# Kernel optimization log

Hardware: AMD Instinct MI355X
Metric: run time of the kernel (lower is better)

## Reference

```python
import jax, jax.numpy as jnp
import numpy as np

B, H, S, D = 2, 16, 2048, 64

def setup_inputs() -> dict:
    key = jax.random.key(0)
    kq, kk, kv = jax.random.split(key, 3)
    Q = jax.random.normal(kq, (B, H, S, D), dtype=jnp.float32)
    K = jax.random.normal(kk, (B, H, S, D), dtype=jnp.float32)
    V = jax.random.normal(kv, (B, H, S, D), dtype=jnp.float32)
    return {"Q": Q, "K": K, "V": V}

def reference(Q, K, V):
    # scores: [B, H, S, S]
    scale = 1.0 / jnp.sqrt(jnp.asarray(Q.shape[-1], Q.dtype))
    scores = jnp.einsum('bhqd,bhkd->bhqk', Q, K) * scale
    probs = jax.nn.softmax(scores, axis=-1)
    out = jnp.einsum('bhqk,bhkd->bhqd', probs, V)
    return out
```

## Files before the change

kernel.cpp:

```cpp
#include <hip/hip_runtime.h>
#include <hip/hip_bf16.h>


#define Bn 2
#define Hn 16
#define Sn 2048
#define Dn 64
#define KP 72
#define OP 68

typedef __attribute__((ext_vector_type(8)))  short s16x8;
typedef __attribute__((ext_vector_type(16))) float f32x16;

__device__ __forceinline__ float fast_exp2(float x) {
#if __has_builtin(__builtin_amdgcn_exp2f)
    return __builtin_amdgcn_exp2f(x);
#else
    return exp2f(x);
#endif
}
__device__ __forceinline__ unsigned short f2bf(float f) {
    unsigned u = __float_as_uint(f);
    return (unsigned short)((u + 0x7fffu + ((u >> 16) & 1u)) >> 16);
}
__device__ __forceinline__ unsigned pack2bf(float lo, float hi) {
    return (unsigned)f2bf(lo) | ((unsigned)f2bf(hi) << 16);
}
__device__ __forceinline__ unsigned packtrunc(float lo, float hi) {
#if __has_builtin(__builtin_amdgcn_perm)
    return __builtin_amdgcn_perm(__float_as_uint(hi), __float_as_uint(lo),
                                 0x07060302u);
#else
    return (__float_as_uint(lo) >> 16) | (__float_as_uint(hi) & 0xffff0000u);
#endif
}
__device__ __forceinline__ s16x8 lds_frag(const unsigned short* p) {
    uint4 u = *(const uint4*)p;
    return __builtin_bit_cast(s16x8, u);
}
__device__ __forceinline__ s16x8 reg_frag(uint4 u) {
    return __builtin_bit_cast(s16x8, u);
}

__global__ __launch_bounds__(256)
void cast_kv2(const float* __restrict__ K, const float* __restrict__ V,
              unsigned short* __restrict__ Kb, unsigned short* __restrict__ Vt) {
    __shared__ unsigned short TK[64 * 72];
    __shared__ unsigned short TV[64 * 72];
    const int tid = threadIdx.x;
    const int bh  = blockIdx.x >> 5;
    const int kt  = blockIdx.x & 31;
    const int r = tid >> 2, cc = (tid & 3) * 16;

    const size_t rowbase = ((size_t)bh * Sn + (size_t)kt * 64 + r) * Dn + cc;
    {
        const float* ks = K + rowbase;
        #pragma unroll
        for (int i = 0; i < 2; ++i) {
            float4 f0 = *(const float4*)(ks + 8 * i);
            float4 f1 = *(const float4*)(ks + 8 * i + 4);
            uint4 w;
            w.x = pack2bf(f0.x, f0.y); w.y = pack2bf(f0.z, f0.w);
            w.z = pack2bf(f1.x, f1.y); w.w = pack2bf(f1.z, f1.w);
            *(uint4*)(TK + r * 72 + cc + 8 * i) = w;
        }
    }
    {
        const float* vs = V + rowbase;
        #pragma unroll
        for (int i = 0; i < 4; ++i) {
            float4 f = *(const float4*)(vs + 4 * i);
            const int d0 = cc + 4 * i;
            TV[(d0 + 0) * 72 + r] = f2bf(f.x);
            TV[(d0 + 1) * 72 + r] = f2bf(f.y);
            TV[(d0 + 2) * 72 + r] = f2bf(f.z);
            TV[(d0 + 3) * 72 + r] = f2bf(f.w);
        }
    }
    __syncthreads();
    unsigned short* kd = Kb + ((size_t)(bh * 32 + kt) * 8) * 512;
    unsigned short* vd = Vt + ((size_t)(bh * 32 + kt) * 8) * 512;
    #pragma unroll
    for (int i = 0; i < 2; ++i) {
        const int u = i * 256 + tid;
        const int c = u >> 6, lane = u & 63;
        const int l31 = lane & 31, hf = lane >> 5;
        const int sub = c >> 2, ks = c & 3;
        const int off = (sub * 32 + l31) * 72 + ks * 16 + hf * 8;
        *(uint4*)(kd + c * 512 + lane * 8) = *(const uint4*)(TK + off);
        *(uint4*)(vd + c * 512 + lane * 8) = *(const uint4*)(TV + off);
    }
}

__global__ __launch_bounds__(128, 2)
void attn_fwd_mfma4(const float* __restrict__ Q,
                    const unsigned short* __restrict__ Kb,
                    const unsigned short* __restrict__ Vt,
                    float* __restrict__ O) {
    __shared__ __align__(16) char smem[18432];
    unsigned short* PT = (unsigned short*)smem;
    float* ob = (float*)smem;
    float* lb = ob + 64 * OP;

    const int tid  = threadIdx.x;
    const int wave = tid >> 6;
    const int lane = tid & 63;
    const int l31  = lane & 31;
    const int half = lane >> 5;

    const int bh = blockIdx.x & 31;
    const int q0 = (blockIdx.x >> 5) * 64;

    const float* Qb = Q + ((size_t)bh * Sn + q0) * Dn;
    const float FCT = 0.18033688011112042f;

    s16x8 qf[2][4];
    #pragma unroll
    for (int s = 0; s < 2; ++s) {
        const float* qp = Qb + (size_t)(s * 32 + l31) * Dn;
        #pragma unroll
        for (int ks = 0; ks < 4; ++ks) {
            const int d0 = ks * 16 + half * 8;
            float4 f0 = *(const float4*)(qp + d0);
            float4 f1 = *(const float4*)(qp + d0 + 4);
            uint4 u;
            u.x = pack2bf(f0.x * FCT, f0.y * FCT);
            u.y = pack2bf(f0.z * FCT, f0.w * FCT);
            u.z = pack2bf(f1.x * FCT, f1.y * FCT);
            u.w = pack2bf(f1.z * FCT, f1.w * FCT);
            qf[s][ks] = __builtin_bit_cast(s16x8, u);
        }
    }

    f32x16 acc00, acc01, acc10, acc11;
    #pragma unroll
    for (int r = 0; r < 16; ++r) { acc00[r]=0.f; acc01[r]=0.f; acc10[r]=0.f; acc11[r]=0.f; }
    float l0 = 0.f, l1 = 0.f;

    const unsigned short* kbase =
        Kb + ((size_t)(bh * 32 + wave * 16) * 8) * 512 + (size_t)lane * 8;
    const unsigned short* vbase =
        Vt + ((size_t)(bh * 32 + wave * 16) * 8) * 512 + (size_t)lane * 8;

    unsigned short* ptw0 = PT + ((size_t)wave * 64 + l31) * KP;
    unsigned short* ptw1 = ptw0 + 32 * KP;

    uint4 kbuf[2][8], vv[8];
    #pragma unroll
    for (int c = 0; c < 8; ++c)
        kbuf[0][c] = *(const uint4*)(kbase + c * 512);

    #pragma unroll
    for (int t = 0; t < 16; ++t) {
        uint4* CUR = kbuf[t & 1];
        uint4* NXT = kbuf[(t + 1) & 1];
        #pragma unroll
        for (int c = 0; c < 8; ++c)
            vv[c] = *(const uint4*)(vbase + (size_t)(t * 8 + c) * 512);
        const int tk = (t < 15 ? t + 1 : 15);
        #pragma unroll
        for (int c = 0; c < 8; ++c)
            NXT[c] = *(const uint4*)(kbase + (size_t)(tk * 8 + c) * 512);

        #pragma unroll
        for (int s = 0; s < 2; ++s) {
            f32x16 c0, c1;
            #pragma unroll
            for (int r = 0; r < 16; ++r) { c0[r] = 0.f; c1[r] = 0.f; }
            __builtin_amdgcn_s_setprio(1);
            #pragma unroll
            for (int ks = 0; ks < 4; ++ks) {
                c0 = __builtin_amdgcn_mfma_f32_32x32x16_bf16(reg_frag(CUR[ks]),     qf[s][ks], c0, 0, 0, 0);
                c1 = __builtin_amdgcn_mfma_f32_32x32x16_bf16(reg_frag(CUR[4 + ks]), qf[s][ks], c1, 0, 0, 0);
            }
            __builtin_amdgcn_s_setprio(0);
            #pragma unroll
            for (int r = 0; r < 16; ++r) {
                c0[r] = fast_exp2(c0[r]);
                c1[r] = fast_exp2(c1[r]);
            }
            float a0 = 0.f, a1 = 0.f, a2 = 0.f, a3 = 0.f;
            #pragma unroll
            for (int r = 0; r < 16; r += 4) {
                a0 += c0[r] + c1[r];
                a1 += c0[r + 1] + c1[r + 1];
                a2 += c0[r + 2] + c1[r + 2];
                a3 += c0[r + 3] + c1[r + 3];
            }
            if (s == 0) l0 += (a0 + a1) + (a2 + a3);
            else        l1 += (a0 + a1) + (a2 + a3);

            unsigned short* ptw = s ? ptw1 : ptw0;
            #pragma unroll
            for (int g = 0; g < 4; ++g) {
                uint2 w0, w1;
                w0.x = packtrunc(c0[4 * g + 0], c0[4 * g + 1]);
                w0.y = packtrunc(c0[4 * g + 2], c0[4 * g + 3]);
                w1.x = packtrunc(c1[4 * g + 0], c1[4 * g + 1]);
                w1.y = packtrunc(c1[4 * g + 2], c1[4 * g + 3]);
                *(uint2*)(ptw + 8 * g + 4 * half)      = w0;
                *(uint2*)(ptw + 8 * g + 4 * half + 32) = w1;
            }
        }

        __builtin_amdgcn_s_setprio(1);
        #pragma unroll
        for (int ks = 0; ks < 4; ++ks) {
            const int off = ks * 16 + half * 8;
            s16x8 pf0 = lds_frag(ptw0 + off);
            s16x8 pf1 = lds_frag(ptw1 + off);
            s16x8 va  = reg_frag(vv[ks]);
            s16x8 vb  = reg_frag(vv[4 + ks]);
            acc00 = __builtin_amdgcn_mfma_f32_32x32x16_bf16(va, pf0, acc00, 0, 0, 0);
            acc01 = __builtin_amdgcn_mfma_f32_32x32x16_bf16(vb, pf0, acc01, 0, 0, 0);
            acc10 = __builtin_amdgcn_mfma_f32_32x32x16_bf16(va, pf1, acc10, 0, 0, 0);
            acc11 = __builtin_amdgcn_mfma_f32_32x32x16_bf16(vb, pf1, acc11, 0, 0, 0);
        }
        __builtin_amdgcn_s_setprio(0);
    }

    l0 += __shfl_xor(l0, 32, 64);
    l1 += __shfl_xor(l1, 32, 64);

    __syncthreads();
    if (wave == 0) {
        #pragma unroll
        for (int g = 0; g < 4; ++g) {
            const int d0 = 8 * g + 4 * half;
            float4 f;
            f.x = acc00[4*g+0]; f.y = acc00[4*g+1]; f.z = acc00[4*g+2]; f.w = acc00[4*g+3];
            *(float4*)(ob + l31 * OP + d0) = f;
            f.x = acc01[4*g+0]; f.y = acc01[4*g+1]; f.z = acc01[4*g+2]; f.w = acc01[4*g+3];
            *(float4*)(ob + l31 * OP + d0 + 32) = f;
            f.x = acc10[4*g+0]; f.y = acc10[4*g+1]; f.z = acc10[4*g+2]; f.w = acc10[4*g+3];
            *(float4*)(ob + (32 + l31) * OP + d0) = f;
            f.x = acc11[4*g+0]; f.y = acc11[4*g+1]; f.z = acc11[4*g+2]; f.w = acc11[4*g+3];
            *(float4*)(ob + (32 + l31) * OP + d0 + 32) = f;
        }
        if (half == 0) { lb[l31] = l0; lb[32 + l31] = l1; }
    }
    __syncthreads();
    if (wave == 1) {
        const float i0 = 1.0f / (l0 + lb[l31]);
        const float i1 = 1.0f / (l1 + lb[32 + l31]);
        #pragma unroll
        for (int g = 0; g < 4; ++g) {
            const int d0 = 8 * g + 4 * half;
            float4 f;
            float* p;
            p = ob + l31 * OP + d0;            f = *(float4*)p;
            f.x = (f.x + acc00[4*g+0]) * i0; f.y = (f.y + acc00[4*g+1]) * i0;
            f.z = (f.z + acc00[4*g+2]) * i0; f.w = (f.w + acc00[4*g+3]) * i0;
            *(float4*)p = f;
            p = ob + l31 * OP + d0 + 32;       f = *(float4*)p;
            f.x = (f.x + acc01[4*g+0]) * i0; f.y = (f.y + acc01[4*g+1]) * i0;
            f.z = (f.z + acc01[4*g+2]) * i0; f.w = (f.w + acc01[4*g+3]) * i0;
            *(float4*)p = f;
            p = ob + (32 + l31) * OP + d0;     f = *(float4*)p;
            f.x = (f.x + acc10[4*g+0]) * i1; f.y = (f.y + acc10[4*g+1]) * i1;
            f.z = (f.z + acc10[4*g+2]) * i1; f.w = (f.w + acc10[4*g+3]) * i1;
            *(float4*)p = f;
            p = ob + (32 + l31) * OP + d0 + 32; f = *(float4*)p;
            f.x = (f.x + acc11[4*g+0]) * i1; f.y = (f.y + acc11[4*g+1]) * i1;
            f.z = (f.z + acc11[4*g+2]) * i1; f.w = (f.w + acc11[4*g+3]) * i1;
            *(float4*)p = f;
        }
    }
    __syncthreads();
    float* op = O + ((size_t)bh * Sn + q0) * Dn;
    #pragma unroll
    for (int it = 0; it < 8; ++it) {
        const int idx = it * 128 + tid;
        const int r = idx >> 4, c4 = (idx & 15) * 4;
        *(float4*)(op + r * Dn + c4) = *(float4*)(ob + r * OP + c4);
    }
}

extern "C" void kernel_launch(void* const* d_in, const int* in_sizes, int n_in,
                              void* d_out, int out_size, void* d_ws, size_t ws_size,
                              hipStream_t stream) {
    const float* Q = (const float*)d_in[0];
    const float* K = (const float*)d_in[1];
    const float* V = (const float*)d_in[2];
    float* O = (float*)d_out;

    const size_t elems = (size_t)Bn * Hn * Sn * Dn;
    unsigned short* Kb = (unsigned short*)d_ws;
    unsigned short* Vt = Kb + elems;

    cast_kv2<<<dim3(Bn * Hn * (Sn / 64)), dim3(256), 0, stream>>>(K, V, Kb, Vt);
    attn_fwd_mfma4<<<dim3(Bn * Hn * (Sn / 64)), dim3(128), 0, stream>>>(Q, Kb, Vt, O);
}
```

Measured before the change: 130.9 us.

## Split key range across four waves per block with LDS reduction

Each block now runs four waves instead of two, and each wave handles one eighth of the key tiles instead of half. The partial outputs and row sums are reduced through a larger shared buffer: two staging buffers, pairwise adds, and a final combine-and-normalize during the store. The first score MFMA now takes a zero vector directly instead of a zero-initialized accumulator. The aim is more parallelism per query tile and shorter serial loops, at the cost of more shared memory, an extra reduction stage, and a tighter register budget from the launch bounds of 256 threads with 4 blocks.

```diff
diff --git a/kernel.cpp b/kernel.cpp
--- a/kernel.cpp
+++ b/kernel.cpp
@@ -92,15 +92,16 @@
     }
 }
 
-__global__ __launch_bounds__(128, 2)
+__global__ __launch_bounds__(256, 4)
 void attn_fwd_mfma4(const float* __restrict__ Q,
                     const unsigned short* __restrict__ Kb,
                     const unsigned short* __restrict__ Vt,
                     float* __restrict__ O) {
-    __shared__ __align__(16) char smem[18432];
+    __shared__ __align__(16) char smem[36864];
     unsigned short* PT = (unsigned short*)smem;
-    float* ob = (float*)smem;
-    float* lb = ob + 64 * OP;
+    float* ob0 = (float*)smem;
+    float* ob1 = ob0 + 64 * OP;
+    float* lb  = ob0 + 2 * 64 * OP;
 
     const int tid  = threadIdx.x;
     const int wave = tid >> 6;
@@ -132,15 +133,19 @@
         }
     }
 
+    f32x16 Z16;
+    #pragma unroll
+    for (int r = 0; r < 16; ++r) Z16[r] = 0.f;
+
     f32x16 acc00, acc01, acc10, acc11;
     #pragma unroll
     for (int r = 0; r < 16; ++r) { acc00[r]=0.f; acc01[r]=0.f; acc10[r]=0.f; acc11[r]=0.f; }
     float l0 = 0.f, l1 = 0.f;
 
     const unsigned short* kbase =
-        Kb + ((size_t)(bh * 32 + wave * 16) * 8) * 512 + (size_t)lane * 8;
+        Kb + ((size_t)(bh * 32 + wave * 8) * 8) * 512 + (size_t)lane * 8;
     const unsigned short* vbase =
-        Vt + ((size_t)(bh * 32 + wave * 16) * 8) * 512 + (size_t)lane * 8;
+        Vt + ((size_t)(bh * 32 + wave * 8) * 8) * 512 + (size_t)lane * 8;
 
     unsigned short* ptw0 = PT + ((size_t)wave * 64 + l31) * KP;
     unsigned short* ptw1 = ptw0 + 32 * KP;
@@ -151,25 +156,24 @@
         kbuf[0][c] = *(const uint4*)(kbase + c * 512);
 
     #pragma unroll
-    for (int t = 0; t < 16; ++t) {
+    for (int t = 0; t < 8; ++t) {
         uint4* CUR = kbuf[t & 1];
         uint4* NXT = kbuf[(t + 1) & 1];
         #pragma unroll
         for (int c = 0; c < 8; ++c)
             vv[c] = *(const uint4*)(vbase + (size_t)(t * 8 + c) * 512);
-        const int tk = (t < 15 ? t + 1 : 15);
+        const int tk = (t < 7 ? t + 1 : 7);
         #pragma unroll
         for (int c = 0; c < 8; ++c)
             NXT[c] = *(const uint4*)(kbase + (size_t)(tk * 8 + c) * 512);
 
         #pragma unroll
         for (int s = 0; s < 2; ++s) {
-            f32x16 c0, c1;
+            __builtin_amdgcn_s_setprio(1);
+            f32x16 c0 = __builtin_amdgcn_mfma_f32_32x32x16_bf16(reg_frag(CUR[0]), qf[s][0], Z16, 0, 0, 0);
+            f32x16 c1 = __builtin_amdgcn_mfma_f32_32x32x16_bf16(reg_frag(CUR[4]), qf[s][0], Z16, 0, 0, 0);
             #pragma unroll
-            for (int r = 0; r < 16; ++r) { c0[r] = 0.f; c1[r] = 0.f; }
-            __builtin_amdgcn_s_setprio(1);
-            #pragma unroll
-            for (int ks = 0; ks < 4; ++ks) {
+            for (int ks = 1; ks < 4; ++ks) {
                 c0 = __builtin_amdgcn_mfma_f32_32x32x16_bf16(reg_frag(CUR[ks]),     qf[s][ks], c0, 0, 0, 0);
                 c1 = __builtin_amdgcn_mfma_f32_32x32x16_bf16(reg_frag(CUR[4 + ks]), qf[s][ks], c1, 0, 0, 0);
             }
@@ -223,56 +227,64 @@
     l1 += __shfl_xor(l1, 32, 64);
 
     __syncthreads();
-    if (wave == 0) {
+    if (half == 0) {
+        lb[wave * 64 + l31]      = l0;
+        lb[wave * 64 + 32 + l31] = l1;
+    }
+    float* obw = (wave & 2) ? ob1 : ob0;
+    if (!(wave & 1)) {
         #pragma unroll
         for (int g = 0; g < 4; ++g) {
             const int d0 = 8 * g + 4 * half;
             float4 f;
             f.x = acc00[4*g+0]; f.y = acc00[4*g+1]; f.z = acc00[4*g+2]; f.w = acc00[4*g+3];
-            *(float4*)(ob + l31 * OP + d0) = f;
+            *(float4*)(obw + l31 * OP + d0) = f;
             f.x = acc01[4*g+0]; f.y = acc01[4*g+1]; f.z = acc01[4*g+2]; f.w = acc01[4*g+3];
-            *(float4*)(ob + l31 * OP + d0 + 32) = f;
+            *(float4*)(obw + l31 * OP + d0 + 32) = f;
             f.x = acc10[4*g+0]; f.y = acc10[4*g+1]; f.z = acc10[4*g+2]; f.w = acc10[4*g+3];
-            *(float4*)(ob + (32 + l31) * OP + d0) = f;
+            *(float4*)(obw + (32 + l31) * OP + d0) = f;
             f.x = acc11[4*g+0]; f.y = acc11[4*g+1]; f.z = acc11[4*g+2]; f.w = acc11[4*g+3];
-            *(float4*)(ob + (32 + l31) * OP + d0 + 32) = f;
-        }
-        if (half == 0) { lb[l31] = l0; lb[32 + l31] = l1; }
+            *(float4*)(obw + (32 + l31) * OP + d0 + 32) = f;
+        }
     }
     __syncthreads();
-    if (wave == 1) {
-        const float i0 = 1.0f / (l0 + lb[l31]);
-        const float i1 = 1.0f / (l1 + lb[32 + l31]);
+    if (wave & 1) {
         #pragma unroll
         for (int g = 0; g < 4; ++g) {
             const int d0 = 8 * g + 4 * half;
             float4 f;
             float* p;
-            p = ob + l31 * OP + d0;            f = *(float4*)p;
-            f.x = (f.x + acc00[4*g+0]) * i0; f.y = (f.y + acc00[4*g+1]) * i0;
-            f.z = (f.z + acc00[4*g+2]) * i0; f.w = (f.w + acc00[4*g+3]) * i0;
+            p = obw + l31 * OP + d0;            f = *(float4*)p;
+            f.x += acc00[4*g+0]; f.y += acc00[4*g+1];
+            f.z += acc00[4*g+2]; f.w += acc00[4*g+3];
             *(float4*)p = f;
-            p = ob + l31 * OP + d0 + 32;       f = *(float4*)p;
-            f.x = (f.x + acc01[4*g+0]) * i0; f.y = (f.y + acc01[4*g+1]) * i0;
-            f.z = (f.z + acc01[4*g+2]) * i0; f.w = (f.w + acc01[4*g+3]) * i0;
+            p = obw + l31 * OP + d0 + 32;       f = *(float4*)p;
+            f.x += acc01[4*g+0]; f.y += acc01[4*g+1];
+            f.z += acc01[4*g+2]; f.w += acc01[4*g+3];
             *(float4*)p = f;
-            p = ob + (32 + l31) * OP + d0;     f = *(float4*)p;
-            f.x = (f.x + acc10[4*g+0]) * i1; f.y = (f.y + acc10[4*g+1]) * i1;
-            f.z = (f.z + acc10[4*g+2]) * i1; f.w = (f.w + acc10[4*g+3]) * i1;
+            p = obw + (32 + l31) * OP + d0;     f = *(float4*)p;
+            f.x += acc10[4*g+0]; f.y += acc10[4*g+1];
+            f.z += acc10[4*g+2]; f.w += acc10[4*g+3];
             *(float4*)p = f;
-            p = ob + (32 + l31) * OP + d0 + 32; f = *(float4*)p;
-            f.x = (f.x + acc11[4*g+0]) * i1; f.y = (f.y + acc11[4*g+1]) * i1;
-            f.z = (f.z + acc11[4*g+2]) * i1; f.w = (f.w + acc11[4*g+3]) * i1;
+            p = obw + (32 + l31) * OP + d0 + 32; f = *(float4*)p;
+            f.x += acc11[4*g+0]; f.y += acc11[4*g+1];
+            f.z += acc11[4*g+2]; f.w += acc11[4*g+3];
             *(float4*)p = f;
         }
     }
     __syncthreads();
     float* op = O + ((size_t)bh * Sn + q0) * Dn;
     #pragma unroll
-    for (int it = 0; it < 8; ++it) {
-        const int idx = it * 128 + tid;
+    for (int it = 0; it < 4; ++it) {
+        const int idx = it * 256 + tid;
         const int r = idx >> 4, c4 = (idx & 15) * 4;
-        *(float4*)(op + r * Dn + c4) = *(float4*)(ob + r * OP + c4);
+        const float inv = 1.0f / (lb[r] + lb[64 + r] + lb[128 + r] + lb[192 + r]);
+        float4 a = *(float4*)(ob0 + r * OP + c4);
+        float4 b = *(float4*)(ob1 + r * OP + c4);
+        float4 f;
+        f.x = (a.x + b.x) * inv; f.y = (a.y + b.y) * inv;
+        f.z = (a.z + b.z) * inv; f.w = (a.w + b.w) * inv;
+        *(float4*)(op + r * Dn + c4) = f;
     }
 }
 
@@ -289,5 +301,5 @@
     unsigned short* Vt = Kb + elems;
 
     cast_kv2<<<dim3(Bn * Hn * (Sn / 64)), dim3(256), 0, stream>>>(K, V, Kb, Vt);
-    attn_fwd_mfma4<<<dim3(Bn * Hn * (Sn / 64)), dim3(128), 0, stream>>>(Q, Kb, Vt, O);
-}
+    attn_fwd_mfma4<<<dim3(Bn * Hn * (Sn / 64)), dim3(256), 0, stream>>>(Q, Kb, Vt, O);
+}
```

Measured after the change: 331.3 us. 2.53x slower.

## Halve query tile to 32 rows per block, doubling grid and occupancy

Applied to the files above, without the earlier changes.

Each block now handles 32 query rows instead of 64, so the grid doubles and per-block LDS and accumulator registers halve. Launch bounds are raised to allow 4 blocks per SM, and the K double-buffer prefetch is replaced by a per-iteration load. Normalisation moves into the final store loop. Each K/V tile loaded from memory now feeds half as many MFMAs, so global and L2 traffic for K/V doubles in exchange for more waves to hide latency.

```diff
diff --git a/kernel.cpp b/kernel.cpp
--- a/kernel.cpp
+++ b/kernel.cpp
@@ -92,15 +92,15 @@
     }
 }
 
-__global__ __launch_bounds__(128, 2)
+__global__ __launch_bounds__(128, 4)
 void attn_fwd_mfma4(const float* __restrict__ Q,
                     const unsigned short* __restrict__ Kb,
                     const unsigned short* __restrict__ Vt,
                     float* __restrict__ O) {
-    __shared__ __align__(16) char smem[18432];
+    __shared__ __align__(16) char smem[9216];
     unsigned short* PT = (unsigned short*)smem;
     float* ob = (float*)smem;
-    float* lb = ob + 64 * OP;
+    float* lb = ob + 32 * OP;
 
     const int tid  = threadIdx.x;
     const int wave = tid >> 6;
@@ -109,15 +109,14 @@
     const int half = lane >> 5;
 
     const int bh = blockIdx.x & 31;
-    const int q0 = (blockIdx.x >> 5) * 64;
+    const int q0 = (blockIdx.x >> 5) * 32;
 
     const float* Qb = Q + ((size_t)bh * Sn + q0) * Dn;
     const float FCT = 0.18033688011112042f;
 
-    s16x8 qf[2][4];
-    #pragma unroll
-    for (int s = 0; s < 2; ++s) {
-        const float* qp = Qb + (size_t)(s * 32 + l31) * Dn;
+    s16x8 qf[4];
+    {
+        const float* qp = Qb + (size_t)l31 * Dn;
         #pragma unroll
         for (int ks = 0; ks < 4; ++ks) {
             const int d0 = ks * 16 + half * 8;
@@ -128,151 +127,124 @@
             u.y = pack2bf(f0.z * FCT, f0.w * FCT);
             u.z = pack2bf(f1.x * FCT, f1.y * FCT);
             u.w = pack2bf(f1.z * FCT, f1.w * FCT);
-            qf[s][ks] = __builtin_bit_cast(s16x8, u);
-        }
-    }
-
-    f32x16 acc00, acc01, acc10, acc11;
-    #pragma unroll
-    for (int r = 0; r < 16; ++r) { acc00[r]=0.f; acc01[r]=0.f; acc10[r]=0.f; acc11[r]=0.f; }
-    float l0 = 0.f, l1 = 0.f;
+            qf[ks] = __builtin_bit_cast(s16x8, u);
+        }
+    }
+
+    f32x16 acc0, acc1;
+    #pragma unroll
+    for (int r = 0; r < 16; ++r) { acc0[r] = 0.f; acc1[r] = 0.f; }
+    float l0 = 0.f;
 
     const unsigned short* kbase =
         Kb + ((size_t)(bh * 32 + wave * 16) * 8) * 512 + (size_t)lane * 8;
     const unsigned short* vbase =
         Vt + ((size_t)(bh * 32 + wave * 16) * 8) * 512 + (size_t)lane * 8;
 
-    unsigned short* ptw0 = PT + ((size_t)wave * 64 + l31) * KP;
-    unsigned short* ptw1 = ptw0 + 32 * KP;
-
-    uint4 kbuf[2][8], vv[8];
-    #pragma unroll
-    for (int c = 0; c < 8; ++c)
-        kbuf[0][c] = *(const uint4*)(kbase + c * 512);
+    unsigned short* ptw = PT + ((size_t)(wave * 32 + l31)) * KP;
 
     #pragma unroll
     for (int t = 0; t < 16; ++t) {
-        uint4* CUR = kbuf[t & 1];
-        uint4* NXT = kbuf[(t + 1) & 1];
+        uint4 kk[8];
+        #pragma unroll
+        for (int c = 0; c < 8; ++c)
+            kk[c] = *(const uint4*)(kbase + (size_t)(t * 8 + c) * 512);
+
+        f32x16 c0, c1;
+        #pragma unroll
+        for (int r = 0; r < 16; ++r) { c0[r] = 0.f; c1[r] = 0.f; }
+        __builtin_amdgcn_s_setprio(1);
+        #pragma unroll
+        for (int ks = 0; ks < 4; ++ks) {
+            c0 = __builtin_amdgcn_mfma_f32_32x32x16_bf16(reg_frag(kk[ks]),     qf[ks], c0, 0, 0, 0);
+            c1 = __builtin_amdgcn_mfma_f32_32x32x16_bf16(reg_frag(kk[4 + ks]), qf[ks], c1, 0, 0, 0);
+        }
+        __builtin_amdgcn_s_setprio(0);
+
+        uint4 vv[8];
         #pragma unroll
         for (int c = 0; c < 8; ++c)
             vv[c] = *(const uint4*)(vbase + (size_t)(t * 8 + c) * 512);
-        const int tk = (t < 15 ? t + 1 : 15);
-        #pragma unroll
-        for (int c = 0; c < 8; ++c)
-            NXT[c] = *(const uint4*)(kbase + (size_t)(tk * 8 + c) * 512);
-
-        #pragma unroll
-        for (int s = 0; s < 2; ++s) {
-            f32x16 c0, c1;
-            #pragma unroll
-            for (int r = 0; r < 16; ++r) { c0[r] = 0.f; c1[r] = 0.f; }
-            __builtin_amdgcn_s_setprio(1);
-            #pragma unroll
-            for (int ks = 0; ks < 4; ++ks) {
-                c0 = __builtin_amdgcn_mfma_f32_32x32x16_bf16(reg_frag(CUR[ks]),     qf[s][ks], c0, 0, 0, 0);
-                c1 = __builtin_amdgcn_mfma_f32_32x32x16_bf16(reg_frag(CUR[4 + ks]), qf[s][ks], c1, 0, 0, 0);
-            }
-            __builtin_amdgcn_s_setprio(0);
-            #pragma unroll
-            for (int r = 0; r < 16; ++r) {
-                c0[r] = fast_exp2(c0[r]);
-                c1[r] = fast_exp2(c1[r]);
-            }
-            float a0 = 0.f, a1 = 0.f, a2 = 0.f, a3 = 0.f;
-            #pragma unroll
-            for (int r = 0; r < 16; r += 4) {
-                a0 += c0[r] + c1[r];
-                a1 += c0[r + 1] + c1[r + 1];
-                a2 += c0[r + 2] + c1[r + 2];
-                a3 += c0[r + 3] + c1[r + 3];
-            }
-            if (s == 0) l0 += (a0 + a1) + (a2 + a3);
-            else        l1 += (a0 + a1) + (a2 + a3);
-
-            unsigned short* ptw = s ? ptw1 : ptw0;
-            #pragma unroll
-            for (int g = 0; g < 4; ++g) {
-                uint2 w0, w1;
-                w0.x = packtrunc(c0[4 * g + 0], c0[4 * g + 1]);
-                w0.y = packtrunc(c0[4 * g + 2], c0[4 * g + 3]);
-                w1.x = packtrunc(c1[4 * g + 0], c1[4 * g + 1]);
-                w1.y = packtrunc(c1[4 * g + 2], c1[4 * g + 3]);
-                *(uint2*)(ptw + 8 * g + 4 * half)      = w0;
-                *(uint2*)(ptw + 8 * g + 4 * half + 32) = w1;
-            }
+
+        #pragma unroll
+        for (int r = 0; r < 16; ++r) {
+            c0[r] = fast_exp2(c0[r]);
+            c1[r] = fast_exp2(c1[r]);
+        }
+        float a0 = 0.f, a1 = 0.f, a2 = 0.f, a3 = 0.f;
+        #pragma unroll
+        for (int r = 0; r < 16; r += 4) {
+            a0 += c0[r] + c1[r];
+            a1 += c0[r + 1] + c1[r + 1];
+            a2 += c0[r + 2] + c1[r + 2];
+            a3 += c0[r + 3] + c1[r + 3];
+        }
+        l0 += (a0 + a1) + (a2 + a3);
+
+        #pragma unroll
+        for (int g = 0; g < 4; ++g) {
+            uint2 w0, w1;
+            w0.x = packtrunc(c0[4 * g + 0], c0[4 * g + 1]);
+            w0.y = packtrunc(c0[4 * g + 2], c0[4 * g + 3]);
+            w1.x = packtrunc(c1[4 * g + 0], c1[4 * g + 1]);
+            w1.y = packtrunc(c1[4 * g + 2], c1[4 * g + 3]);
+            *(uint2*)(ptw + 8 * g + 4 * half)      = w0;
+            *(uint2*)(ptw + 8 * g + 4 * half + 32) = w1;
         }
 
         __builtin_amdgcn_s_setprio(1);
         #pragma unroll
         for (int ks = 0; ks < 4; ++ks) {
             const int off = ks * 16 + half * 8;
-            s16x8 pf0 = lds_frag(ptw0 + off);
-            s16x8 pf1 = lds_frag(ptw1 + off);
-            s16x8 va  = reg_frag(vv[ks]);
-            s16x8 vb  = reg_frag(vv[4 + ks]);
-            acc00 = __builtin_amdgcn_mfma_f32_32x32x16_bf16(va, pf0, acc00, 0, 0, 0);
-            acc01 = __builtin_amdgcn_mfma_f32_32x32x16_bf16(vb, pf0, acc01, 0, 0, 0);
-            acc10 = __builtin_amdgcn_mfma_f32_32x32x16_bf16(va, pf1, acc10, 0, 0, 0);
-            acc11 = __builtin_amdgcn_mfma_f32_32x32x16_bf16(vb, pf1, acc11, 0, 0, 0);
+            s16x8 pf = lds_frag(ptw + off);
+            acc0 = __builtin_amdgcn_mfma_f32_32x32x16_bf16(reg_frag(vv[ks]),     pf, acc0, 0, 0, 0);
+            acc1 = __builtin_amdgcn_mfma_f32_32x32x16_bf16(reg_frag(vv[4 + ks]), pf, acc1, 0, 0, 0);
         }
         __builtin_amdgcn_s_setprio(0);
     }
 
     l0 += __shfl_xor(l0, 32, 64);
-    l1 += __shfl_xor(l1, 32, 64);
-
-    __syncthreads();
+
+    __syncthreads();
+    if (half == 0) lb[wave * 32 + l31] = l0;
     if (wave == 0) {
         #pragma unroll
         for (int g = 0; g < 4; ++g) {
             const int d0 = 8 * g + 4 * half;
             float4 f;
-            f.x = acc00[4*g+0]; f.y = acc00[4*g+1]; f.z = acc00[4*g+2]; f.w = acc00[4*g+3];
+            f.x = acc0[4*g+0]; f.y = acc0[4*g+1]; f.z = acc0[4*g+2]; f.w = acc0[4*g+3];
             *(float4*)(ob + l31 * OP + d0) = f;
-            f.x = acc01[4*g+0]; f.y = acc01[4*g+1]; f.z = acc01[4*g+2]; f.w = acc01[4*g+3];
+            f.x = acc1[4*g+0]; f.y = acc1[4*g+1]; f.z = acc1[4*g+2]; f.w = acc1[4*g+3];
             *(float4*)(ob + l31 * OP + d0 + 32) = f;
-            f.x = acc10[4*g+0]; f.y = acc10[4*g+1]; f.z = acc10[4*g+2]; f.w = acc10[4*g+3];
-            *(float4*)(ob + (32 + l31) * OP + d0) = f;
-            f.x = acc11[4*g+0]; f.y = acc11[4*g+1]; f.z = acc11[4*g+2]; f.w = acc11[4*g+3];
-            *(float4*)(ob + (32 + l31) * OP + d0 + 32) = f;
-        }
-        if (half == 0) { lb[l31] = l0; lb[32 + l31] = l1; }
+        }
     }
     __syncthreads();
     if (wave == 1) {
-        const float i0 = 1.0f / (l0 + lb[l31]);
-        const float i1 = 1.0f / (l1 + lb[32 + l31]);
         #pragma unroll
         for (int g = 0; g < 4; ++g) {
             const int d0 = 8 * g + 4 * half;
             float4 f;
             float* p;
-            p = ob + l31 * OP + d0;            f = *(float4*)p;
-            f.x = (f.x + acc00[4*g+0]) * i0; f.y = (f.y + acc00[4*g+1]) * i0;
-            f.z = (f.z + acc00[4*g+2]) * i0; f.w = (f.w + acc00[4*g+3]) * i0;
+            p = ob + l31 * OP + d0;       f = *(float4*)p;
+            f.x += acc0[4*g+0]; f.y += acc0[4*g+1];
+            f.z += acc0[4*g+2]; f.w += acc0[4*g+3];
             *(float4*)p = f;
-            p = ob + l31 * OP + d0 + 32;       f = *(float4*)p;
-            f.x = (f.x + acc01[4*g+0]) * i0; f.y = (f.y + acc01[4*g+1]) * i0;
-            f.z = (f.z + acc01[4*g+2]) * i0; f.w = (f.w + acc01[4*g+3]) * i0;
+            p = ob + l31 * OP + d0 + 32;  f = *(float4*)p;
+            f.x += acc1[4*g+0]; f.y += acc1[4*g+1];
+            f.z += acc1[4*g+2]; f.w += acc1[4*g+3];
             *(float4*)p = f;
-            p = ob + (32 + l31) * OP + d0;     f = *(float4*)p;
-            f.x = (f.x + acc10[4*g+0]) * i1; f.y = (f.y + acc10[4*g+1]) * i1;
-            f.z = (f.z + acc10[4*g+2]) * i1; f.w = (f.w + acc10[4*g+3]) * i1;
-            *(float4*)p = f;
-            p = ob + (32 + l31) * OP + d0 + 32; f = *(float4*)p;
-            f.x = (f.x + acc11[4*g+0]) * i1; f.y = (f.y + acc11[4*g+1]) * i1;
-            f.z = (f.z + acc11[4*g+2]) * i1; f.w = (f.w + acc11[4*g+3]) * i1;
-            *(float4*)p = f;
         }
     }
     __syncthreads();
     float* op = O + ((size_t)bh * Sn + q0) * Dn;
     #pragma unroll
-    for (int it = 0; it < 8; ++it) {
+    for (int it = 0; it < 4; ++it) {
         const int idx = it * 128 + tid;
         const int r = idx >> 4, c4 = (idx & 15) * 4;
-        *(float4*)(op + r * Dn + c4) = *(float4*)(ob + r * OP + c4);
+        const float inv = 1.0f / (lb[r] + lb[32 + r]);
+        float4 f = *(float4*)(ob + r * OP + c4);
+        f.x *= inv; f.y *= inv; f.z *= inv; f.w *= inv;
+        *(float4*)(op + r * Dn + c4) = f;
     }
 }
 
@@ -289,5 +261,5 @@
     unsigned short* Vt = Kb + elems;
 
     cast_kv2<<<dim3(Bn * Hn * (Sn / 64)), dim3(256), 0, stream>>>(K, V, Kb, Vt);
-    attn_fwd_mfma4<<<dim3(Bn * Hn * (Sn / 64)), dim3(128), 0, stream>>>(Q, Kb, Vt, O);
-}
+    attn_fwd_mfma4<<<dim3(Bn * Hn * (Sn / 32)), dim3(128), 0, stream>>>(Q, Kb, Vt, O);
+}
```

Result: slower. 155.9 us (+19.1%).

## Keep P tile in registers via permlane32 swap instead of LDS round-trip

Applied to the files above, without the earlier changes.

Builds the PV-MMA B operand from the QK accumulators directly in registers, using v_cvt_pk_bf16_f32 packing plus permlane32_swap to reshuffle lanes. This replaces the per-tile LDS store and reload of P. It removes LDS traffic and its waits from the inner loop, and shrinks shared memory, which may allow higher occupancy. In exchange it raises register pressure, and P is now rounded rather than truncated to bf16.

```diff
diff --git a/kernel.cpp b/kernel.cpp
--- a/kernel.cpp
+++ b/kernel.cpp
@@ -6,11 +6,11 @@
 #define Hn 16
 #define Sn 2048
 #define Dn 64
-#define KP 72
 #define OP 68
 
 typedef __attribute__((ext_vector_type(8)))  short s16x8;
 typedef __attribute__((ext_vector_type(16))) float f32x16;
+typedef __attribute__((ext_vector_type(2)))  unsigned u32x2;
 
 __device__ __forceinline__ float fast_exp2(float x) {
 #if __has_builtin(__builtin_amdgcn_exp2f)
@@ -26,20 +26,30 @@
 __device__ __forceinline__ unsigned pack2bf(float lo, float hi) {
     return (unsigned)f2bf(lo) | ((unsigned)f2bf(hi) << 16);
 }
-__device__ __forceinline__ unsigned packtrunc(float lo, float hi) {
-#if __has_builtin(__builtin_amdgcn_perm)
-    return __builtin_amdgcn_perm(__float_as_uint(hi), __float_as_uint(lo),
-                                 0x07060302u);
-#else
-    return (__float_as_uint(lo) >> 16) | (__float_as_uint(hi) & 0xffff0000u);
-#endif
-}
-__device__ __forceinline__ s16x8 lds_frag(const unsigned short* p) {
-    uint4 u = *(const uint4*)p;
-    return __builtin_bit_cast(s16x8, u);
+__device__ __forceinline__ unsigned cvtpk(float lo, float hi) {
+    unsigned r;
+    asm("v_cvt_pk_bf16_f32 %0, %1, %2" : "=v"(r) : "v"(lo), "v"(hi));
+    return r;
 }
 __device__ __forceinline__ s16x8 reg_frag(uint4 u) {
     return __builtin_bit_cast(s16x8, u);
+}
+
+__device__ __forceinline__ void build_pf(const f32x16& c, uint4& fA, uint4& fB) {
+    unsigned p01 = cvtpk(c[0], c[1]);
+    unsigned p23 = cvtpk(c[2], c[3]);
+    unsigned p45 = cvtpk(c[4], c[5]);
+    unsigned p67 = cvtpk(c[6], c[7]);
+    u32x2 s0 = __builtin_amdgcn_permlane32_swap(p01, p45, false, false);
+    u32x2 s1 = __builtin_amdgcn_permlane32_swap(p23, p67, false, false);
+    fA.x = s0[0]; fA.y = s1[0]; fA.z = s0[1]; fA.w = s1[1];
+    unsigned p89 = cvtpk(c[8], c[9]);
+    unsigned pab = cvtpk(c[10], c[11]);
+    unsigned pcd = cvtpk(c[12], c[13]);
+    unsigned pef = cvtpk(c[14], c[15]);
+    u32x2 s2 = __builtin_amdgcn_permlane32_swap(p89, pcd, false, false);
+    u32x2 s3 = __builtin_amdgcn_permlane32_swap(pab, pef, false, false);
+    fB.x = s2[0]; fB.y = s3[0]; fB.z = s2[1]; fB.w = s3[1];
 }
 
 __global__ __launch_bounds__(256)
@@ -97,8 +107,7 @@
                     const unsigned short* __restrict__ Kb,
                     const unsigned short* __restrict__ Vt,
                     float* __restrict__ O) {
-    __shared__ __align__(16) char smem[18432];
-    unsigned short* PT = (unsigned short*)smem;
+    __shared__ __align__(16) char smem[64 * OP * 4 + 256];
     float* ob = (float*)smem;
     float* lb = ob + 64 * OP;
 
@@ -142,10 +151,7 @@
     const unsigned short* vbase =
         Vt + ((size_t)(bh * 32 + wave * 16) * 8) * 512 + (size_t)lane * 8;
 
-    unsigned short* ptw0 = PT + ((size_t)wave * 64 + l31) * KP;
-    unsigned short* ptw1 = ptw0 + 32 * KP;
-
-    uint4 kbuf[2][8], vv[8];
+    uint4 kbuf[2][8];
     #pragma unroll
     for (int c = 0; c < 8; ++c)
         kbuf[0][c] = *(const uint4*)(kbase + c * 512);
@@ -154,6 +160,8 @@
     for (int t = 0; t < 16; ++t) {
         uint4* CUR = kbuf[t & 1];
         uint4* NXT = kbuf[(t + 1) & 1];
+
+        uint4 vv[8];
         #pragma unroll
         for (int c = 0; c < 8; ++c)
             vv[c] = *(const uint4*)(vbase + (size_t)(t * 8 + c) * 512);
@@ -162,16 +170,18 @@
         for (int c = 0; c < 8; ++c)
             NXT[c] = *(const uint4*)(kbase + (size_t)(tk * 8 + c) * 512);
 
-        #pragma unroll
-        for (int s = 0; s < 2; ++s) {
+        uint4 p00, p01, p02, p03;
+        uint4 p10, p11, p12, p13;
+
+        {
             f32x16 c0, c1;
             #pragma unroll
             for (int r = 0; r < 16; ++r) { c0[r] = 0.f; c1[r] = 0.f; }
             __builtin_amdgcn_s_setprio(1);
             #pragma unroll
             for (int ks = 0; ks < 4; ++ks) {
-                c0 = __builtin_amdgcn_mfma_f32_32x32x16_bf16(reg_frag(CUR[ks]),     qf[s][ks], c0, 0, 0, 0);
-                c1 = __builtin_amdgcn_mfma_f32_32x32x16_bf16(reg_frag(CUR[4 + ks]), qf[s][ks], c1, 0, 0, 0);
+                c0 = __builtin_amdgcn_mfma_f32_32x32x16_bf16(reg_frag(CUR[ks]),     qf[0][ks], c0, 0, 0, 0);
+                c1 = __builtin_amdgcn_mfma_f32_32x32x16_bf16(reg_frag(CUR[4 + ks]), qf[0][ks], c1, 0, 0, 0);
             }
             __builtin_amdgcn_s_setprio(0);
             #pragma unroll
@@ -187,35 +197,57 @@
                 a2 += c0[r + 2] + c1[r + 2];
                 a3 += c0[r + 3] + c1[r + 3];
             }
-            if (s == 0) l0 += (a0 + a1) + (a2 + a3);
-            else        l1 += (a0 + a1) + (a2 + a3);
-
-            unsigned short* ptw = s ? ptw1 : ptw0;
-            #pragma unroll
-            for (int g = 0; g < 4; ++g) {
-                uint2 w0, w1;
-                w0.x = packtrunc(c0[4 * g + 0], c0[4 * g + 1]);
-                w0.y = packtrunc(c0[4 * g + 2], c0[4 * g + 3]);
-                w1.x = packtrunc(c1[4 * g + 0], c1[4 * g + 1]);
-                w1.y = packtrunc(c1[4 * g + 2], c1[4 * g + 3]);
-                *(uint2*)(ptw + 8 * g + 4 * half)      = w0;
-                *(uint2*)(ptw + 8 * g + 4 * half + 32) = w1;
-            }
+            l0 += (a0 + a1) + (a2 + a3);
+            build_pf(c0, p00, p01);
+            build_pf(c1, p02, p03);
+        }
+
+        {
+            f32x16 c0, c1;
+            #pragma unroll
+            for (int r = 0; r < 16; ++r) { c0[r] = 0.f; c1[r] = 0.f; }
+            __builtin_amdgcn_s_setprio(1);
+            #pragma unroll
+            for (int ks = 0; ks < 4; ++ks) {
+                c0 = __builtin_amdgcn_mfma_f32_32x32x16_bf16(reg_frag(CUR[ks]),     qf[1][ks], c0, 0, 0, 0);
+                c1 = __builtin_amdgcn_mfma_f32_32x32x16_bf16(reg_frag(CUR[4 + ks]), qf[1][ks], c1, 0, 0, 0);
+            }
+            __builtin_amdgcn_s_setprio(0);
+            #pragma unroll
+            for (int r = 0; r < 16; ++r) {
+                c0[r] = fast_exp2(c0[r]);
+                c1[r] = fast_exp2(c1[r]);
+            }
+            float a0 = 0.f, a1 = 0.f, a2 = 0.f, a3 = 0.f;
+            #pragma unroll
+            for (int r = 0; r < 16; r += 4) {
+                a0 += c0[r] + c1[r];
+                a1 += c0[r + 1] + c1[r + 1];
+                a2 += c0[r + 2] + c1[r + 2];
+                a3 += c0[r + 3] + c1[r + 3];
+            }
+            l1 += (a0 + a1) + (a2 + a3);
+            build_pf(c0, p10, p11);
+            build_pf(c1, p12, p13);
         }
 
         __builtin_amdgcn_s_setprio(1);
-        #pragma unroll
-        for (int ks = 0; ks < 4; ++ks) {
-            const int off = ks * 16 + half * 8;
-            s16x8 pf0 = lds_frag(ptw0 + off);
-            s16x8 pf1 = lds_frag(ptw1 + off);
-            s16x8 va  = reg_frag(vv[ks]);
-            s16x8 vb  = reg_frag(vv[4 + ks]);
-            acc00 = __builtin_amdgcn_mfma_f32_32x32x16_bf16(va, pf0, acc00, 0, 0, 0);
-            acc01 = __builtin_amdgcn_mfma_f32_32x32x16_bf16(vb, pf0, acc01, 0, 0, 0);
-            acc10 = __builtin_amdgcn_mfma_f32_32x32x16_bf16(va, pf1, acc10, 0, 0, 0);
-            acc11 = __builtin_amdgcn_mfma_f32_32x32x16_bf16(vb, pf1, acc11, 0, 0, 0);
-        }
+        acc00 = __builtin_amdgcn_mfma_f32_32x32x16_bf16(reg_frag(vv[0]), reg_frag(p00), acc00, 0, 0, 0);
+        acc01 = __builtin_amdgcn_mfma_f32_32x32x16_bf16(reg_frag(vv[4]), reg_frag(p00), acc01, 0, 0, 0);
+        acc10 = __builtin_amdgcn_mfma_f32_32x32x16_bf16(reg_frag(vv[0]), reg_frag(p10), acc10, 0, 0, 0);
+        acc11 = __builtin_amdgcn_mfma_f32_32x32x16_bf16(reg_frag(vv[4]), reg_frag(p10), acc11, 0, 0, 0);
+        acc00 = __builtin_amdgcn_mfma_f32_32x32x16_bf16(reg_frag(vv[1]), reg_frag(p01), acc00, 0, 0, 0);
+        acc01 = __builtin_amdgcn_mfma_f32_32x32x16_bf16(reg_frag(vv[5]), reg_frag(p01), acc01, 0, 0, 0);
+        acc10 = __builtin_amdgcn_mfma_f32_32x32x16_bf16(reg_frag(vv[1]), reg_frag(p11), acc10, 0, 0, 0);
+        acc11 = __builtin_amdgcn_mfma_f32_32x32x16_bf16(reg_frag(vv[5]), reg_frag(p11), acc11, 0, 0, 0);
+        acc00 = __builtin_amdgcn_mfma_f32_32x32x16_bf16(reg_frag(vv[2]), reg_frag(p02), acc00, 0, 0, 0);
+        acc01 = __builtin_amdgcn_mfma_f32_32x32x16_bf16(reg_frag(vv[6]), reg_frag(p02), acc01, 0, 0, 0);
+        acc10 = __builtin_amdgcn_mfma_f32_32x32x16_bf16(reg_frag(vv[2]), reg_frag(p12), acc10, 0, 0, 0);
+        acc11 = __builtin_amdgcn_mfma_f32_32x32x16_bf16(reg_frag(vv[6]), reg_frag(p12), acc11, 0, 0, 0);
+        acc00 = __builtin_amdgcn_mfma_f32_32x32x16_bf16(reg_frag(vv[3]), reg_frag(p03), acc00, 0, 0, 0);
+        acc01 = __builtin_amdgcn_mfma_f32_32x32x16_bf16(reg_frag(vv[7]), reg_frag(p03), acc01, 0, 0, 0);
+        acc10 = __builtin_amdgcn_mfma_f32_32x32x16_bf16(reg_frag(vv[3]), reg_frag(p13), acc10, 0, 0, 0);
+        acc11 = __builtin_amdgcn_mfma_f32_32x32x16_bf16(reg_frag(vv[7]), reg_frag(p13), acc11, 0, 0, 0);
         __builtin_amdgcn_s_setprio(0);
     }
 
```

After: 130.0 us (median of 2 runs). About the same (-0.7%).
